# Kernel tuning notes

Hardware: AMD Instinct MI355X
Metric: run time of the kernel (lower is better)

The kernel has to match this reference:

```python
import jax, jax.numpy as jnp
import numpy as np

N, B, H, OUT, T = 200000, 1024, 256, 128, 2  # nodes, graphs, hidden(=in_dim), out_dim, timesteps
NEG_SLOPE = 0.01


def setup_inputs() -> dict:
    key = jax.random.key(0)
    ks = jax.random.split(key, 12)
    s = 0.05
    f32 = jnp.float32
    return {
        "x": jax.random.normal(ks[0], (N, H), dtype=f32),
        "batch": jnp.sort(jax.random.randint(ks[1], (N,), 0, B)),
        # GATConv params (heads=1, shared lin for src/dst since in_channels is int)
        "W": jax.random.normal(ks[2], (H, H), dtype=f32) * s,
        "att_src": jax.random.normal(ks[3], (H,), dtype=f32) * s,
        "att_dst": jax.random.normal(ks[4], (H,), dtype=f32) * s,
        "bias_gat": jnp.zeros((H,), dtype=f32),
        # GRUCell params (input_size = H, hidden_size = H)
        "W_ih": jax.random.normal(ks[5], (3 * H, H), dtype=f32) * s,
        "W_hh": jax.random.normal(ks[6], (3 * H, H), dtype=f32) * s,
        "b_ih": jnp.zeros((3 * H,), dtype=f32),
        "b_hh": jnp.zeros((3 * H,), dtype=f32),
        # final Linear
        "W_lin": jax.random.normal(ks[7], (H, OUT), dtype=f32) * s,
        "b_lin": jnp.zeros((OUT,), dtype=f32),
    }


def reference(x, batch, W, att_src, att_dst, bias_gat, W_ih, W_hh, b_ih, b_hh, W_lin, b_lin):
    # out = global_add_pool(x, batch)  -> [B, H]
    out = jax.ops.segment_sum(x, batch, num_segments=B)
    for _ in range(T):
        # --- bipartite GATConv((x, out), edge_index=[arange(N), batch]) ---
        xs = x @ W                       # [N, H] transformed source nodes
        od = out @ W                     # [B, H] transformed dst (graph) nodes
        a_src = xs @ att_src             # [N]
        a_dst = od @ att_dst             # [B]
        e = a_src + a_dst[batch]         # [N] per-edge raw score (one edge per node)
        e = jnp.where(e > 0, e, NEG_SLOPE * e)  # leaky_relu(negative_slope=0.01)
        # scatter-softmax over each graph's incoming edges
        emax = jax.ops.segment_max(e, batch, num_segments=B)
        ee = jnp.exp(e - emax[batch])
        denom = jax.ops.segment_sum(ee, batch, num_segments=B)
        alpha = ee / denom[batch]        # [N]
        # scatter-add aggregation of weighted messages
        agg = jax.ops.segment_sum(xs * alpha[:, None], batch, num_segments=B) + bias_gat
        h = jax.nn.elu(agg)              # [B, H]  (dropout is identity in eval)
        # --- GRUCell(h, out) ---
        gi = h @ W_ih.T + b_ih           # [B, 3H]
        gh = out @ W_hh.T + b_hh         # [B, 3H]
        r = jax.nn.sigmoid(gi[:, :H] + gh[:, :H])
        z = jax.nn.sigmoid(gi[:, H:2 * H] + gh[:, H:2 * H])
        n = jnp.tanh(gi[:, 2 * H:] + r * gh[:, 2 * H:])
        out = jax.nn.silu((1.0 - z) * n + z * out)  # activation = F.silu
    return out @ W_lin + b_lin           # [B, OUT]
```

## Files before the change

kernel.cpp:

```cpp
#include <hip/hip_runtime.h>
#include <math.h>

#define N_NODES 200000
#define BGRAPH  1024
#define HDIM    256
#define ODIM    128
#define SCAP    1024

typedef __attribute__((ext_vector_type(8))) short short8;
typedef __attribute__((ext_vector_type(4))) float f32x4;

__device__ __forceinline__ unsigned short f2bf(float f) {
    union { float f; unsigned int i; } c; c.f = f;
    unsigned int i = c.i;
    unsigned int r = i + 0x7FFFu + ((i >> 16) & 1u);
    return (unsigned short)(r >> 16);
}

__global__ __launch_bounds__(256) void k_prep(const float* __restrict__ W,
        const float* __restrict__ att_src, const float* __restrict__ att_dst,
        const int* __restrict__ batch, float* __restrict__ v, float* __restrict__ u,
        int* __restrict__ seg) {
    int t = threadIdx.x;
    if (blockIdx.x < 256) {
        int i = blockIdx.x;
        float w = W[(size_t)i * HDIM + t];
        __shared__ float r1[256], r2[256];
        r1[t] = w * att_src[t];
        r2[t] = w * att_dst[t];
        __syncthreads();
        for (int st = 128; st > 0; st >>= 1) {
            if (t < st) { r1[t] += r1[t + st]; r2[t] += r2[t + st]; }
            __syncthreads();
        }
        if (t == 0) { v[i] = r1[0]; u[i] = r2[0]; }
    } else {
        int b = (blockIdx.x - 256) * 256 + t;
        if (b > BGRAPH) return;
        if (b == BGRAPH) { seg[b] = N_NODES; return; }
        int lo = 0, hi = N_NODES;
        while (lo < hi) { int mid = (lo + hi) >> 1; if (batch[mid] < b) lo = mid + 1; else hi = mid; }
        seg[b] = lo;
    }
}

__global__ __launch_bounds__(256) void k_passAB(const float* __restrict__ x,
        const int* __restrict__ seg, const float* __restrict__ v,
        const float* __restrict__ u, const float* __restrict__ W,
        const float* __restrict__ bias_gat,
        float* __restrict__ s, float* __restrict__ smax,
        float* __restrict__ stt, float* __restrict__ hbuf) {
    int b = blockIdx.x;
    int lo = seg[b], hi = seg[b + 1];
    int t = threadIdx.x, wave = t >> 6, lane = t & 63;
    float v0 = v[4 * lane + 0], v1 = v[4 * lane + 1], v2 = v[4 * lane + 2], v3 = v[4 * lane + 3];
    __shared__ float s_loc[SCAP];
    __shared__ float comb[4][HDIM];
    __shared__ float red[256];
    __shared__ float sred[4], dred[4];
    bool inl = (hi - lo) <= SCAP;

    float p0 = 0.f, p1 = 0.f, p2 = 0.f, p3 = 0.f;
    float sm = -3.402823466e38f;
    int i = lo + wave;
    for (; i + 4 < hi; i += 8) {
        const float4 r0 = *(const float4*)(x + (size_t)i * HDIM + 4 * lane);
        const float4 r1 = *(const float4*)(x + (size_t)(i + 4) * HDIM + 4 * lane);
        p0 += r0.x + r1.x; p1 += r0.y + r1.y; p2 += r0.z + r1.z; p3 += r0.w + r1.w;
        float pa = r0.x * v0 + r0.y * v1 + r0.z * v2 + r0.w * v3;
        float pb = r1.x * v0 + r1.y * v1 + r1.z * v2 + r1.w * v3;
        #pragma unroll
        for (int off = 32; off > 0; off >>= 1) {
            pa += __shfl_down(pa, off, 64);
            pb += __shfl_down(pb, off, 64);
        }
        if (lane == 0) {
            s[i] = pa; s[i + 4] = pb;
            if (inl) { s_loc[i - lo] = pa; s_loc[i + 4 - lo] = pb; }
            sm = fmaxf(sm, fmaxf(pa, pb));
        }
    }
    for (; i < hi; i += 4) {
        const float4 r0 = *(const float4*)(x + (size_t)i * HDIM + 4 * lane);
        p0 += r0.x; p1 += r0.y; p2 += r0.z; p3 += r0.w;
        float pa = r0.x * v0 + r0.y * v1 + r0.z * v2 + r0.w * v3;
        #pragma unroll
        for (int off = 32; off > 0; off >>= 1) pa += __shfl_down(pa, off, 64);
        if (lane == 0) {
            s[i] = pa;
            if (inl) s_loc[i - lo] = pa;
            sm = fmaxf(sm, pa);
        }
    }
    comb[wave][4 * lane + 0] = p0; comb[wave][4 * lane + 1] = p1;
    comb[wave][4 * lane + 2] = p2; comb[wave][4 * lane + 3] = p3;
    if (lane == 0) sred[wave] = sm;
    __syncthreads();
    float st0 = comb[0][t] + comb[1][t] + comb[2][t] + comb[3][t];
    stt[(size_t)b * HDIM + t] = st0;
    float smx = fmaxf(fmaxf(sred[0], sred[1]), fmaxf(sred[2], sred[3]));
    if (t == 0) smax[b] = smx;
    red[t] = st0 * u[t];
    __syncthreads();
    for (int st = 128; st > 0; st >>= 1) { if (t < st) red[t] += red[t + st]; __syncthreads(); }
    float d1 = red[0];
    __syncthreads();
    float M = smx + d1;
    M = M > 0.f ? M : 0.01f * M;

    float a0 = 0.f, a1 = 0.f, a2 = 0.f, a3 = 0.f, den = 0.f;
    i = lo + wave;
    for (; i + 12 < hi; i += 16) {
        float s0v = inl ? s_loc[i - lo]      : s[i];
        float s1v = inl ? s_loc[i + 4 - lo]  : s[i + 4];
        float s2v = inl ? s_loc[i + 8 - lo]  : s[i + 8];
        float s3v = inl ? s_loc[i + 12 - lo] : s[i + 12];
        float e0 = s0v + d1; e0 = e0 > 0.f ? e0 : 0.01f * e0;
        float e1 = s1v + d1; e1 = e1 > 0.f ? e1 : 0.01f * e1;
        float e2 = s2v + d1; e2 = e2 > 0.f ? e2 : 0.01f * e2;
        float e3 = s3v + d1; e3 = e3 > 0.f ? e3 : 0.01f * e3;
        float w0 = __expf(e0 - M), w1 = __expf(e1 - M);
        float w2 = __expf(e2 - M), w3 = __expf(e3 - M);
        const float4 r0 = *(const float4*)(x + (size_t)i * HDIM + 4 * lane);
        const float4 r1 = *(const float4*)(x + (size_t)(i + 4) * HDIM + 4 * lane);
        const float4 r2 = *(const float4*)(x + (size_t)(i + 8) * HDIM + 4 * lane);
        const float4 r3 = *(const float4*)(x + (size_t)(i + 12) * HDIM + 4 * lane);
        den += (w0 + w1) + (w2 + w3);
        a0 += w0 * r0.x + w1 * r1.x + w2 * r2.x + w3 * r3.x;
        a1 += w0 * r0.y + w1 * r1.y + w2 * r2.y + w3 * r3.y;
        a2 += w0 * r0.z + w1 * r1.z + w2 * r2.z + w3 * r3.z;
        a3 += w0 * r0.w + w1 * r1.w + w2 * r2.w + w3 * r3.w;
    }
    for (; i < hi; i += 4) {
        float s0v = inl ? s_loc[i - lo] : s[i];
        float e0 = s0v + d1; e0 = e0 > 0.f ? e0 : 0.01f * e0;
        float w0 = __expf(e0 - M);
        const float4 r0 = *(const float4*)(x + (size_t)i * HDIM + 4 * lane);
        den += w0;
        a0 += w0 * r0.x; a1 += w0 * r0.y; a2 += w0 * r0.z; a3 += w0 * r0.w;
    }
    __syncthreads();
    comb[wave][4 * lane + 0] = a0; comb[wave][4 * lane + 1] = a1;
    comb[wave][4 * lane + 2] = a2; comb[wave][4 * lane + 3] = a3;
    if (lane == 0) dred[wave] = den;
    __syncthreads();
    float dtot = dred[0] + dred[1] + dred[2] + dred[3];
    float inv = (hi > lo) ? 1.0f / dtot : 0.f;
    __shared__ float ax[HDIM];
    ax[t] = (comb[0][t] + comb[1][t] + comb[2][t] + comb[3][t]) * inv;
    __syncthreads();
    float acc = bias_gat[t];
    #pragma unroll 8
    for (int ii = 0; ii < HDIM; ++ii) acc += ax[ii] * W[(size_t)ii * HDIM + t];
    hbuf[(size_t)b * HDIM + t] = acc > 0.f ? acc : expm1f(acc);
}

__global__ __launch_bounds__(256) void k_iter2(const float* __restrict__ x,
        const int* __restrict__ seg, const float* __restrict__ s,
        const float* __restrict__ u, const float* __restrict__ smax,
        float* __restrict__ stt,
        const float* __restrict__ gi, const float* __restrict__ gh,
        const float* __restrict__ b_ih, const float* __restrict__ b_hh,
        const float* __restrict__ W, const float* __restrict__ bias_gat,
        float* __restrict__ hbuf) {
    int b = blockIdx.x, t = threadIdx.x;
    int lo = seg[b], hi = seg[b + 1];
    size_t base = (size_t)b * (3 * HDIM);
    float gir = gi[base + t] + b_ih[t];
    float giz = gi[base + HDIM + t] + b_ih[HDIM + t];
    float gin = gi[base + 2 * HDIM + t] + b_ih[2 * HDIM + t];
    float ghr = gh[base + t] + b_hh[t];
    float ghz = gh[base + HDIM + t] + b_hh[HDIM + t];
    float ghn = gh[base + 2 * HDIM + t] + b_hh[2 * HDIM + t];
    float r = 1.f / (1.f + __expf(-(gir + ghr)));
    float z = 1.f / (1.f + __expf(-(giz + ghz)));
    float n = tanhf(gin + r * ghn);
    float prev = stt[(size_t)b * HDIM + t];
    float h2 = (1.f - z) * n + z * prev;
    float st_j = h2 / (1.f + __expf(-h2));
    stt[(size_t)b * HDIM + t] = st_j;

    __shared__ float red[256];
    red[t] = st_j * u[t];
    __syncthreads();
    for (int st = 128; st > 0; st >>= 1) { if (t < st) red[t] += red[t + st]; __syncthreads(); }
    float d2 = red[0];
    __syncthreads();
    float M = smax[b] + d2;
    M = M > 0.f ? M : 0.01f * M;

    int wave = t >> 6, lane = t & 63;
    float a0 = 0.f, a1 = 0.f, a2 = 0.f, a3 = 0.f, den = 0.f;
    int i = lo + wave;
    for (; i + 12 < hi; i += 16) {
        float e0 = s[i] + d2;      e0 = e0 > 0.f ? e0 : 0.01f * e0;
        float e1 = s[i + 4] + d2;  e1 = e1 > 0.f ? e1 : 0.01f * e1;
        float e2 = s[i + 8] + d2;  e2 = e2 > 0.f ? e2 : 0.01f * e2;
        float e3 = s[i + 12] + d2; e3 = e3 > 0.f ? e3 : 0.01f * e3;
        float w0 = __expf(e0 - M), w1 = __expf(e1 - M);
        float w2 = __expf(e2 - M), w3 = __expf(e3 - M);
        const float4 r0 = *(const float4*)(x + (size_t)i * HDIM + 4 * lane);
        const float4 r1 = *(const float4*)(x + (size_t)(i + 4) * HDIM + 4 * lane);
        const float4 r2 = *(const float4*)(x + (size_t)(i + 8) * HDIM + 4 * lane);
        const float4 r3 = *(const float4*)(x + (size_t)(i + 12) * HDIM + 4 * lane);
        den += (w0 + w1) + (w2 + w3);
        a0 += w0 * r0.x + w1 * r1.x + w2 * r2.x + w3 * r3.x;
        a1 += w0 * r0.y + w1 * r1.y + w2 * r2.y + w3 * r3.y;
        a2 += w0 * r0.z + w1 * r1.z + w2 * r2.z + w3 * r3.z;
        a3 += w0 * r0.w + w1 * r1.w + w2 * r2.w + w3 * r3.w;
    }
    for (; i < hi; i += 4) {
        float e0 = s[i] + d2; e0 = e0 > 0.f ? e0 : 0.01f * e0;
        float w0 = __expf(e0 - M);
        const float4 r0 = *(const float4*)(x + (size_t)i * HDIM + 4 * lane);
        den += w0;
        a0 += w0 * r0.x; a1 += w0 * r0.y; a2 += w0 * r0.z; a3 += w0 * r0.w;
    }
    __shared__ float comb[4][HDIM];
    __shared__ float dred[4];
    comb[wave][4 * lane + 0] = a0; comb[wave][4 * lane + 1] = a1;
    comb[wave][4 * lane + 2] = a2; comb[wave][4 * lane + 3] = a3;
    if (lane == 0) dred[wave] = den;
    __syncthreads();
    float dtot = dred[0] + dred[1] + dred[2] + dred[3];
    float inv = (hi > lo) ? 1.0f / dtot : 0.f;
    __shared__ float ax[HDIM];
    ax[t] = (comb[0][t] + comb[1][t] + comb[2][t] + comb[3][t]) * inv;
    __syncthreads();
    float acc = bias_gat[t];
    #pragma unroll 8
    for (int ii = 0; ii < HDIM; ++ii) acc += ax[ii] * W[(size_t)ii * HDIM + t];
    hbuf[(size_t)b * HDIM + t] = acc > 0.f ? acc : expm1f(acc);
}

__global__ __launch_bounds__(256) void k_gemm2m(const float* __restrict__ A0,
        const float* __restrict__ A1, const float* __restrict__ B0,
        const float* __restrict__ B1, float* __restrict__ C0, float* __restrict__ C1) {
    const int K = HDIM, N = 3 * HDIM;
    const float* A = blockIdx.z ? A1 : A0;
    const float* Bm = blockIdx.z ? B1 : B0;
    float* C = blockIdx.z ? C1 : C0;
    int m0 = blockIdx.x * 64, n0 = blockIdx.y * 64;
    __shared__ __align__(16) unsigned short As[64][40];
    __shared__ __align__(16) unsigned short Bs[64][40];
    int t = threadIdx.x;
    int wave = t >> 6, lane = t & 63;
    int quad = lane >> 4, l16 = lane & 15;
    f32x4 acc[4] = {};
    for (int k0 = 0; k0 < K; k0 += 32) {
        int r = t >> 2;
        int kq = (t & 3) << 3;
        float4 av0 = *(const float4*)(A + (size_t)(m0 + r) * K + k0 + kq);
        float4 av1 = *(const float4*)(A + (size_t)(m0 + r) * K + k0 + kq + 4);
        short8 pa;
        pa[0] = (short)f2bf(av0.x); pa[1] = (short)f2bf(av0.y);
        pa[2] = (short)f2bf(av0.z); pa[3] = (short)f2bf(av0.w);
        pa[4] = (short)f2bf(av1.x); pa[5] = (short)f2bf(av1.y);
        pa[6] = (short)f2bf(av1.z); pa[7] = (short)f2bf(av1.w);
        *(short8*)&As[r][kq] = pa;
        float4 bv0 = *(const float4*)(Bm + (size_t)(n0 + r) * K + k0 + kq);
        float4 bv1 = *(const float4*)(Bm + (size_t)(n0 + r) * K + k0 + kq + 4);
        short8 pb;
        pb[0] = (short)f2bf(bv0.x); pb[1] = (short)f2bf(bv0.y);
        pb[2] = (short)f2bf(bv0.z); pb[3] = (short)f2bf(bv0.w);
        pb[4] = (short)f2bf(bv1.x); pb[5] = (short)f2bf(bv1.y);
        pb[6] = (short)f2bf(bv1.z); pb[7] = (short)f2bf(bv1.w);
        *(short8*)&Bs[r][kq] = pb;
        __syncthreads();
        short8 a = *(const short8*)&As[wave * 16 + l16][quad * 8];
        #pragma unroll
        for (int tn = 0; tn < 4; ++tn) {
            short8 bfr = *(const short8*)&Bs[tn * 16 + l16][quad * 8];
            acc[tn] = __builtin_amdgcn_mfma_f32_16x16x32_bf16(a, bfr, acc[tn], 0, 0, 0);
        }
        __syncthreads();
    }
    #pragma unroll
    for (int tn = 0; tn < 4; ++tn)
        #pragma unroll
        for (int rr = 0; rr < 4; ++rr)
            C[(size_t)(m0 + wave * 16 + quad * 4 + rr) * N + n0 + tn * 16 + l16] = acc[tn][rr];
}

__global__ __launch_bounds__(256) void k_final(const float* __restrict__ gi,
        const float* __restrict__ gh, const float* __restrict__ b_ih,
        const float* __restrict__ b_hh, const float* __restrict__ stt,
        const float* __restrict__ B, const float* __restrict__ bias,
        float* __restrict__ C, int M, int N, int K) {
    __shared__ __align__(16) float As[16][64];
    __shared__ __align__(16) float Bs[16][64];
    int tx = threadIdx.x & 15, ty = threadIdx.x >> 4;
    int m0 = blockIdx.x * 64, n0 = blockIdx.y * 64;
    float acc[4][4] = {};
    for (int k0 = 0; k0 < K; k0 += 16) {
        {
            int r = threadIdx.x >> 2;
            int kk0 = (threadIdx.x & 3) << 2;
            int mrow = m0 + r;
            size_t base = (size_t)mrow * (3 * HDIM);
            #pragma unroll
            for (int q = 0; q < 4; ++q) {
                int k = k0 + kk0 + q;
                float gir = gi[base + k] + b_ih[k];
                float giz = gi[base + HDIM + k] + b_ih[HDIM + k];
                float gin = gi[base + 2 * HDIM + k] + b_ih[2 * HDIM + k];
                float ghr = gh[base + k] + b_hh[k];
                float ghz = gh[base + HDIM + k] + b_hh[HDIM + k];
                float ghn = gh[base + 2 * HDIM + k] + b_hh[2 * HDIM + k];
                float rg = 1.f / (1.f + __expf(-(gir + ghr)));
                float zg = 1.f / (1.f + __expf(-(giz + ghz)));
                float ng = tanhf(gin + rg * ghn);
                float prev = stt[(size_t)mrow * HDIM + k];
                float h2 = (1.f - zg) * ng + zg * prev;
                As[kk0 + q][r] = h2 / (1.f + __expf(-h2));
            }
        }
        {
            int kk = threadIdx.x >> 4;
            int nn = (threadIdx.x & 15) << 2;
            float4 bv = *(const float4*)(B + (size_t)(k0 + kk) * N + n0 + nn);
            Bs[kk][nn + 0] = bv.x; Bs[kk][nn + 1] = bv.y;
            Bs[kk][nn + 2] = bv.z; Bs[kk][nn + 3] = bv.w;
        }
        __syncthreads();
        #pragma unroll
        for (int kk = 0; kk < 16; ++kk) {
            float4 a = *(const float4*)&As[kk][ty * 4];
            float4 bb = *(const float4*)&Bs[kk][tx * 4];
            acc[0][0] += a.x * bb.x; acc[0][1] += a.x * bb.y; acc[0][2] += a.x * bb.z; acc[0][3] += a.x * bb.w;
            acc[1][0] += a.y * bb.x; acc[1][1] += a.y * bb.y; acc[1][2] += a.y * bb.z; acc[1][3] += a.y * bb.w;
            acc[2][0] += a.z * bb.x; acc[2][1] += a.z * bb.y; acc[2][2] += a.z * bb.z; acc[2][3] += a.z * bb.w;
            acc[3][0] += a.w * bb.x; acc[3][1] += a.w * bb.y; acc[3][2] += a.w * bb.z; acc[3][3] += a.w * bb.w;
        }
        __syncthreads();
    }
    float bsv[4];
    #pragma unroll
    for (int j = 0; j < 4; ++j) bsv[j] = bias[n0 + tx * 4 + j];
    #pragma unroll
    for (int i = 0; i < 4; ++i) {
        int mrow = m0 + ty * 4 + i;
        *(float4*)(C + (size_t)mrow * N + n0 + tx * 4) =
            make_float4(acc[i][0] + bsv[0], acc[i][1] + bsv[1],
                        acc[i][2] + bsv[2], acc[i][3] + bsv[3]);
    }
}

extern "C" void kernel_launch(void* const* d_in, const int* in_sizes, int n_in,
                              void* d_out, int out_size, void* d_ws, size_t ws_size,
                              hipStream_t stream) {
    const float* x        = (const float*)d_in[0];
    const int*   batch    = (const int*)d_in[1];
    const float* W        = (const float*)d_in[2];
    const float* att_src  = (const float*)d_in[3];
    const float* att_dst  = (const float*)d_in[4];
    const float* bias_gat = (const float*)d_in[5];
    const float* W_ih     = (const float*)d_in[6];
    const float* W_hh     = (const float*)d_in[7];
    const float* b_ih     = (const float*)d_in[8];
    const float* b_hh     = (const float*)d_in[9];
    const float* W_lin    = (const float*)d_in[10];
    const float* b_lin    = (const float*)d_in[11];

    char* ws = (char*)d_ws;
    size_t off = 0;
    auto alloc = [&](size_t bytes) {
        void* p = (void*)(ws + off);
        off += (bytes + 255) & ~(size_t)255;
        return p;
    };
    int*   seg  = (int*)alloc((BGRAPH + 1) * 4);
    float* vv   = (float*)alloc(HDIM * 4);
    float* uu   = (float*)alloc(HDIM * 4);
    float* smax = (float*)alloc(BGRAPH * 4);
    float* s    = (float*)alloc((size_t)N_NODES * 4);
    float* stt  = (float*)alloc((size_t)BGRAPH * HDIM * 4);
    float* hbuf = (float*)alloc((size_t)BGRAPH * HDIM * 4);
    float* gi   = (float*)alloc((size_t)BGRAPH * 3 * HDIM * 4);
    float* gh   = (float*)alloc((size_t)BGRAPH * 3 * HDIM * 4);

    hipLaunchKernelGGL(k_prep, dim3(261), dim3(256), 0, stream,
                       W, att_src, att_dst, batch, vv, uu, seg);
    hipLaunchKernelGGL(k_passAB, dim3(BGRAPH), dim3(256), 0, stream,
                       x, seg, vv, uu, W, bias_gat, s, smax, stt, hbuf);
    hipLaunchKernelGGL(k_gemm2m, dim3(BGRAPH / 64, (3 * HDIM) / 64, 2), dim3(256), 0,
                       stream, hbuf, stt, W_ih, W_hh, gi, gh);
    hipLaunchKernelGGL(k_iter2, dim3(BGRAPH), dim3(256), 0, stream,
                       x, seg, s, uu, smax, stt, gi, gh, b_ih, b_hh, W, bias_gat, hbuf);
    hipLaunchKernelGGL(k_gemm2m, dim3(BGRAPH / 64, (3 * HDIM) / 64, 2), dim3(256), 0,
                       stream, hbuf, stt, W_ih, W_hh, gi, gh);
    hipLaunchKernelGGL(k_final, dim3(BGRAPH / 64, ODIM / 64), dim3(256), 0, stream,
                       gi, gh, b_ih, b_hh, stt, W_lin, b_lin, (float*)d_out,
                       BGRAPH, ODIM, HDIM);
}
```

Before: 480.2 us.

## Fuse both GAT/GRU timesteps and final linear into one per-graph kernel

Collapses the passAB, MFMA GEMM, iter2 and final kernels into a single per-graph kernel that runs both timesteps, the GRU matvecs and the output projection in-block. The GRU weights are pre-packed into an interleaved bf16 layout in the prep kernel, and each thread does scalar dot products against them. The aim is to remove the gi/gh/stt/hbuf global round trips and four kernel launches. In exchange, each block now reads the full packed GRU weights serially with scalar FMAs instead of using MFMA tiles, which costs extra per-block compute and L2 traffic.

```diff
diff --git a/kernel.cpp b/kernel.cpp
--- a/kernel.cpp
+++ b/kernel.cpp
@@ -8,7 +8,6 @@
 #define SCAP    1024
 
 typedef __attribute__((ext_vector_type(8))) short short8;
-typedef __attribute__((ext_vector_type(4))) float f32x4;
 
 __device__ __forceinline__ unsigned short f2bf(float f) {
     union { float f; unsigned int i; } c; c.f = f;
@@ -16,11 +15,17 @@
     unsigned int r = i + 0x7FFFu + ((i >> 16) & 1u);
     return (unsigned short)(r >> 16);
 }
+__device__ __forceinline__ float bf2f(unsigned short h) {
+    union { unsigned int i; float f; } c; c.i = ((unsigned int)h) << 16;
+    return c.f;
+}
 
 __global__ __launch_bounds__(256) void k_prep(const float* __restrict__ W,
         const float* __restrict__ att_src, const float* __restrict__ att_dst,
-        const int* __restrict__ batch, float* __restrict__ v, float* __restrict__ u,
-        int* __restrict__ seg) {
+        const int* __restrict__ batch, const float* __restrict__ W_ih,
+        const float* __restrict__ W_hh, float* __restrict__ v,
+        float* __restrict__ u, int* __restrict__ seg,
+        unsigned short* __restrict__ Wg) {
     int t = threadIdx.x;
     if (blockIdx.x < 256) {
         int i = blockIdx.x;
@@ -34,32 +39,51 @@
             __syncthreads();
         }
         if (t == 0) { v[i] = r1[0]; u[i] = r2[0]; }
-    } else {
+    } else if (blockIdx.x < 261) {
         int b = (blockIdx.x - 256) * 256 + t;
         if (b > BGRAPH) return;
         if (b == BGRAPH) { seg[b] = N_NODES; return; }
         int lo = 0, hi = N_NODES;
         while (lo < hi) { int mid = (lo + hi) >> 1; if (batch[mid] < b) lo = mid + 1; else hi = mid; }
         seg[b] = lo;
-    }
-}
-
-__global__ __launch_bounds__(256) void k_passAB(const float* __restrict__ x,
+    } else {
+        int k = blockIdx.x - 261;
+        short8 w8;
+        #pragma unroll
+        for (int j = 0; j < 3; ++j)
+            w8[j] = (short)f2bf(W_ih[(size_t)(j * HDIM + t) * HDIM + k]);
+        #pragma unroll
+        for (int j = 0; j < 3; ++j)
+            w8[3 + j] = (short)f2bf(W_hh[(size_t)(j * HDIM + t) * HDIM + k]);
+        w8[6] = 0; w8[7] = 0;
+        *(short8*)(Wg + ((size_t)k * HDIM + t) * 8) = w8;
+    }
+}
+
+__global__ __launch_bounds__(256, 4) void k_fused(const float* __restrict__ x,
         const int* __restrict__ seg, const float* __restrict__ v,
         const float* __restrict__ u, const float* __restrict__ W,
-        const float* __restrict__ bias_gat,
-        float* __restrict__ s, float* __restrict__ smax,
-        float* __restrict__ stt, float* __restrict__ hbuf) {
+        const float* __restrict__ bias_gat, const unsigned short* __restrict__ Wg,
+        const float* __restrict__ b_ih, const float* __restrict__ b_hh,
+        const float* __restrict__ W_lin, const float* __restrict__ b_lin,
+        float* __restrict__ sfall, float* __restrict__ out) {
     int b = blockIdx.x;
     int lo = seg[b], hi = seg[b + 1];
     int t = threadIdx.x, wave = t >> 6, lane = t & 63;
-    float v0 = v[4 * lane + 0], v1 = v[4 * lane + 1], v2 = v[4 * lane + 2], v3 = v[4 * lane + 3];
+
     __shared__ float s_loc[SCAP];
     __shared__ float comb[4][HDIM];
     __shared__ float red[256];
+    __shared__ float axv[HDIM];
+    __shared__ float hvec[HDIM];
+    __shared__ float oprev[HDIM];
     __shared__ float sred[4], dred[4];
+
     bool inl = (hi - lo) <= SCAP;
-
+    float ut = u[t];
+
+    float v0 = v[4 * lane + 0], v1 = v[4 * lane + 1];
+    float v2 = v[4 * lane + 2], v3 = v[4 * lane + 3];
     float p0 = 0.f, p1 = 0.f, p2 = 0.f, p3 = 0.f;
     float sm = -3.402823466e38f;
     int i = lo + wave;
@@ -75,8 +99,8 @@
             pb += __shfl_down(pb, off, 64);
         }
         if (lane == 0) {
-            s[i] = pa; s[i + 4] = pb;
             if (inl) { s_loc[i - lo] = pa; s_loc[i + 4 - lo] = pb; }
+            else     { sfall[i] = pa; sfall[i + 4] = pb; }
             sm = fmaxf(sm, fmaxf(pa, pb));
         }
     }
@@ -87,8 +111,7 @@
         #pragma unroll
         for (int off = 32; off > 0; off >>= 1) pa += __shfl_down(pa, off, 64);
         if (lane == 0) {
-            s[i] = pa;
-            if (inl) s_loc[i - lo] = pa;
+            if (inl) s_loc[i - lo] = pa; else sfall[i] = pa;
             sm = fmaxf(sm, pa);
         }
     }
@@ -97,253 +120,112 @@
     if (lane == 0) sred[wave] = sm;
     __syncthreads();
     float st0 = comb[0][t] + comb[1][t] + comb[2][t] + comb[3][t];
-    stt[(size_t)b * HDIM + t] = st0;
+    oprev[t] = st0;
     float smx = fmaxf(fmaxf(sred[0], sred[1]), fmaxf(sred[2], sred[3]));
-    if (t == 0) smax[b] = smx;
-    red[t] = st0 * u[t];
+    red[t] = st0 * ut;
     __syncthreads();
     for (int st = 128; st > 0; st >>= 1) { if (t < st) red[t] += red[t + st]; __syncthreads(); }
-    float d1 = red[0];
-    __syncthreads();
-    float M = smx + d1;
-    M = M > 0.f ? M : 0.01f * M;
-
-    float a0 = 0.f, a1 = 0.f, a2 = 0.f, a3 = 0.f, den = 0.f;
-    i = lo + wave;
-    for (; i + 12 < hi; i += 16) {
-        float s0v = inl ? s_loc[i - lo]      : s[i];
-        float s1v = inl ? s_loc[i + 4 - lo]  : s[i + 4];
-        float s2v = inl ? s_loc[i + 8 - lo]  : s[i + 8];
-        float s3v = inl ? s_loc[i + 12 - lo] : s[i + 12];
-        float e0 = s0v + d1; e0 = e0 > 0.f ? e0 : 0.01f * e0;
-        float e1 = s1v + d1; e1 = e1 > 0.f ? e1 : 0.01f * e1;
-        float e2 = s2v + d1; e2 = e2 > 0.f ? e2 : 0.01f * e2;
-        float e3 = s3v + d1; e3 = e3 > 0.f ? e3 : 0.01f * e3;
-        float w0 = __expf(e0 - M), w1 = __expf(e1 - M);
-        float w2 = __expf(e2 - M), w3 = __expf(e3 - M);
-        const float4 r0 = *(const float4*)(x + (size_t)i * HDIM + 4 * lane);
-        const float4 r1 = *(const float4*)(x + (size_t)(i + 4) * HDIM + 4 * lane);
-        const float4 r2 = *(const float4*)(x + (size_t)(i + 8) * HDIM + 4 * lane);
-        const float4 r3 = *(const float4*)(x + (size_t)(i + 12) * HDIM + 4 * lane);
-        den += (w0 + w1) + (w2 + w3);
-        a0 += w0 * r0.x + w1 * r1.x + w2 * r2.x + w3 * r3.x;
-        a1 += w0 * r0.y + w1 * r1.y + w2 * r2.y + w3 * r3.y;
-        a2 += w0 * r0.z + w1 * r1.z + w2 * r2.z + w3 * r3.z;
-        a3 += w0 * r0.w + w1 * r1.w + w2 * r2.w + w3 * r3.w;
-    }
-    for (; i < hi; i += 4) {
-        float s0v = inl ? s_loc[i - lo] : s[i];
-        float e0 = s0v + d1; e0 = e0 > 0.f ? e0 : 0.01f * e0;
-        float w0 = __expf(e0 - M);
-        const float4 r0 = *(const float4*)(x + (size_t)i * HDIM + 4 * lane);
-        den += w0;
-        a0 += w0 * r0.x; a1 += w0 * r0.y; a2 += w0 * r0.z; a3 += w0 * r0.w;
-    }
-    __syncthreads();
-    comb[wave][4 * lane + 0] = a0; comb[wave][4 * lane + 1] = a1;
-    comb[wave][4 * lane + 2] = a2; comb[wave][4 * lane + 3] = a3;
-    if (lane == 0) dred[wave] = den;
-    __syncthreads();
-    float dtot = dred[0] + dred[1] + dred[2] + dred[3];
-    float inv = (hi > lo) ? 1.0f / dtot : 0.f;
-    __shared__ float ax[HDIM];
-    ax[t] = (comb[0][t] + comb[1][t] + comb[2][t] + comb[3][t]) * inv;
-    __syncthreads();
-    float acc = bias_gat[t];
+    float d = red[0];
+    __syncthreads();
+
+    for (int step = 0; step < 2; ++step) {
+        float M = smx + d;
+        M = M > 0.f ? M : 0.01f * M;
+
+        float a0 = 0.f, a1 = 0.f, a2 = 0.f, a3 = 0.f, den = 0.f;
+        i = lo + wave;
+        for (; i + 12 < hi; i += 16) {
+            float s0v = inl ? s_loc[i - lo]      : sfall[i];
+            float s1v = inl ? s_loc[i + 4 - lo]  : sfall[i + 4];
+            float s2v = inl ? s_loc[i + 8 - lo]  : sfall[i + 8];
+            float s3v = inl ? s_loc[i + 12 - lo] : sfall[i + 12];
+            float e0 = s0v + d; e0 = e0 > 0.f ? e0 : 0.01f * e0;
+            float e1 = s1v + d; e1 = e1 > 0.f ? e1 : 0.01f * e1;
+            float e2 = s2v + d; e2 = e2 > 0.f ? e2 : 0.01f * e2;
+            float e3 = s3v + d; e3 = e3 > 0.f ? e3 : 0.01f * e3;
+            float w0 = __expf(e0 - M), w1 = __expf(e1 - M);
+            float w2 = __expf(e2 - M), w3 = __expf(e3 - M);
+            const float4 r0 = *(const float4*)(x + (size_t)i * HDIM + 4 * lane);
+            const float4 r1 = *(const float4*)(x + (size_t)(i + 4) * HDIM + 4 * lane);
+            const float4 r2 = *(const float4*)(x + (size_t)(i + 8) * HDIM + 4 * lane);
+            const float4 r3 = *(const float4*)(x + (size_t)(i + 12) * HDIM + 4 * lane);
+            den += (w0 + w1) + (w2 + w3);
+            a0 += w0 * r0.x + w1 * r1.x + w2 * r2.x + w3 * r3.x;
+            a1 += w0 * r0.y + w1 * r1.y + w2 * r2.y + w3 * r3.y;
+            a2 += w0 * r0.z + w1 * r1.z + w2 * r2.z + w3 * r3.z;
+            a3 += w0 * r0.w + w1 * r1.w + w2 * r2.w + w3 * r3.w;
+        }
+        for (; i < hi; i += 4) {
+            float s0v = inl ? s_loc[i - lo] : sfall[i];
+            float e0 = s0v + d; e0 = e0 > 0.f ? e0 : 0.01f * e0;
+            float w0 = __expf(e0 - M);
+            const float4 r0 = *(const float4*)(x + (size_t)i * HDIM + 4 * lane);
+            den += w0;
+            a0 += w0 * r0.x; a1 += w0 * r0.y; a2 += w0 * r0.z; a3 += w0 * r0.w;
+        }
+        comb[wave][4 * lane + 0] = a0; comb[wave][4 * lane + 1] = a1;
+        comb[wave][4 * lane + 2] = a2; comb[wave][4 * lane + 3] = a3;
+        if (lane == 0) dred[wave] = den;
+        __syncthreads();
+        float dtot = dred[0] + dred[1] + dred[2] + dred[3];
+        float inv = (hi > lo) ? 1.0f / dtot : 0.f;
+        axv[t] = (comb[0][t] + comb[1][t] + comb[2][t] + comb[3][t]) * inv;
+        __syncthreads();
+
+        float acc = bias_gat[t];
+        #pragma unroll 8
+        for (int ii = 0; ii < HDIM; ++ii) acc += axv[ii] * W[(size_t)ii * HDIM + t];
+        float hval = acc > 0.f ? acc : expm1f(acc);
+        __syncthreads();
+        hvec[t] = hval;
+        __syncthreads();
+
+        float gr = 0.f, gz = 0.f, gn = 0.f, hr = 0.f, hz = 0.f, hn = 0.f;
+        for (int k0 = 0; k0 < HDIM; k0 += 4) {
+            float hq[4], oq[4];
+            *(float4*)hq = *(const float4*)&hvec[k0];
+            *(float4*)oq = *(const float4*)&oprev[k0];
+            #pragma unroll
+            for (int j = 0; j < 4; ++j) {
+                short8 wv = *(const short8*)(Wg + ((size_t)(k0 + j) * HDIM + t) * 8);
+                gr += hq[j] * bf2f((unsigned short)wv[0]);
+                gz += hq[j] * bf2f((unsigned short)wv[1]);
+                gn += hq[j] * bf2f((unsigned short)wv[2]);
+                hr += oq[j] * bf2f((unsigned short)wv[3]);
+                hz += oq[j] * bf2f((unsigned short)wv[4]);
+                hn += oq[j] * bf2f((unsigned short)wv[5]);
+            }
+        }
+        float gir = gr + b_ih[t];
+        float giz = gz + b_ih[HDIM + t];
+        float gin = gn + b_ih[2 * HDIM + t];
+        float ghr = hr + b_hh[t];
+        float ghz = hz + b_hh[HDIM + t];
+        float ghn = hn + b_hh[2 * HDIM + t];
+        float rg = 1.f / (1.f + __expf(-(gir + ghr)));
+        float zg = 1.f / (1.f + __expf(-(giz + ghz)));
+        float ng = tanhf(gin + rg * ghn);
+        float prev = oprev[t];
+        float h2 = (1.f - zg) * ng + zg * prev;
+        float no = h2 / (1.f + __expf(-h2));
+        __syncthreads();
+        oprev[t] = no;
+        red[t] = no * ut;
+        __syncthreads();
+        for (int st = 128; st > 0; st >>= 1) { if (t < st) red[t] += red[t + st]; __syncthreads(); }
+        d = red[0];
+        __syncthreads();
+    }
+
+    int half = t >> 7, o = t & 127;
+    float acc = 0.f;
     #pragma unroll 8
-    for (int ii = 0; ii < HDIM; ++ii) acc += ax[ii] * W[(size_t)ii * HDIM + t];
-    hbuf[(size_t)b * HDIM + t] = acc > 0.f ? acc : expm1f(acc);
-}
-
-__global__ __launch_bounds__(256) void k_iter2(const float* __restrict__ x,
-        const int* __restrict__ seg, const float* __restrict__ s,
-        const float* __restrict__ u, const float* __restrict__ smax,
-        float* __restrict__ stt,
-        const float* __restrict__ gi, const float* __restrict__ gh,
-        const float* __restrict__ b_ih, const float* __restrict__ b_hh,
-        const float* __restrict__ W, const float* __restrict__ bias_gat,
-        float* __restrict__ hbuf) {
-    int b = blockIdx.x, t = threadIdx.x;
-    int lo = seg[b], hi = seg[b + 1];
-    size_t base = (size_t)b * (3 * HDIM);
-    float gir = gi[base + t] + b_ih[t];
-    float giz = gi[base + HDIM + t] + b_ih[HDIM + t];
-    float gin = gi[base + 2 * HDIM + t] + b_ih[2 * HDIM + t];
-    float ghr = gh[base + t] + b_hh[t];
-    float ghz = gh[base + HDIM + t] + b_hh[HDIM + t];
-    float ghn = gh[base + 2 * HDIM + t] + b_hh[2 * HDIM + t];
-    float r = 1.f / (1.f + __expf(-(gir + ghr)));
-    float z = 1.f / (1.f + __expf(-(giz + ghz)));
-    float n = tanhf(gin + r * ghn);
-    float prev = stt[(size_t)b * HDIM + t];
-    float h2 = (1.f - z) * n + z * prev;
-    float st_j = h2 / (1.f + __expf(-h2));
-    stt[(size_t)b * HDIM + t] = st_j;
-
-    __shared__ float red[256];
-    red[t] = st_j * u[t];
-    __syncthreads();
-    for (int st = 128; st > 0; st >>= 1) { if (t < st) red[t] += red[t + st]; __syncthreads(); }
-    float d2 = red[0];
-    __syncthreads();
-    float M = smax[b] + d2;
-    M = M > 0.f ? M : 0.01f * M;
-
-    int wave = t >> 6, lane = t & 63;
-    float a0 = 0.f, a1 = 0.f, a2 = 0.f, a3 = 0.f, den = 0.f;
-    int i = lo + wave;
-    for (; i + 12 < hi; i += 16) {
-        float e0 = s[i] + d2;      e0 = e0 > 0.f ? e0 : 0.01f * e0;
-        float e1 = s[i + 4] + d2;  e1 = e1 > 0.f ? e1 : 0.01f * e1;
-        float e2 = s[i + 8] + d2;  e2 = e2 > 0.f ? e2 : 0.01f * e2;
-        float e3 = s[i + 12] + d2; e3 = e3 > 0.f ? e3 : 0.01f * e3;
-        float w0 = __expf(e0 - M), w1 = __expf(e1 - M);
-        float w2 = __expf(e2 - M), w3 = __expf(e3 - M);
-        const float4 r0 = *(const float4*)(x + (size_t)i * HDIM + 4 * lane);
-        const float4 r1 = *(const float4*)(x + (size_t)(i + 4) * HDIM + 4 * lane);
-        const float4 r2 = *(const float4*)(x + (size_t)(i + 8) * HDIM + 4 * lane);
-        const float4 r3 = *(const float4*)(x + (size_t)(i + 12) * HDIM + 4 * lane);
-        den += (w0 + w1) + (w2 + w3);
-        a0 += w0 * r0.x + w1 * r1.x + w2 * r2.x + w3 * r3.x;
-        a1 += w0 * r0.y + w1 * r1.y + w2 * r2.y + w3 * r3.y;
-        a2 += w0 * r0.z + w1 * r1.z + w2 * r2.z + w3 * r3.z;
-        a3 += w0 * r0.w + w1 * r1.w + w2 * r2.w + w3 * r3.w;
-    }
-    for (; i < hi; i += 4) {
-        float e0 = s[i] + d2; e0 = e0 > 0.f ? e0 : 0.01f * e0;
-        float w0 = __expf(e0 - M);
-        const float4 r0 = *(const float4*)(x + (size_t)i * HDIM + 4 * lane);
-        den += w0;
-        a0 += w0 * r0.x; a1 += w0 * r0.y; a2 += w0 * r0.z; a3 += w0 * r0.w;
-    }
-    __shared__ float comb[4][HDIM];
-    __shared__ float dred[4];
-    comb[wave][4 * lane + 0] = a0; comb[wave][4 * lane + 1] = a1;
-    comb[wave][4 * lane + 2] = a2; comb[wave][4 * lane + 3] = a3;
-    if (lane == 0) dred[wave] = den;
-    __syncthreads();
-    float dtot = dred[0] + dred[1] + dred[2] + dred[3];
-    float inv = (hi > lo) ? 1.0f / dtot : 0.f;
-    __shared__ float ax[HDIM];
-    ax[t] = (comb[0][t] + comb[1][t] + comb[2][t] + comb[3][t]) * inv;
-    __syncthreads();
-    float acc = bias_gat[t];
-    #pragma unroll 8
-    for (int ii = 0; ii < HDIM; ++ii) acc += ax[ii] * W[(size_t)ii * HDIM + t];
-    hbuf[(size_t)b * HDIM + t] = acc > 0.f ? acc : expm1f(acc);
-}
-
-__global__ __launch_bounds__(256) void k_gemm2m(const float* __restrict__ A0,
-        const float* __restrict__ A1, const float* __restrict__ B0,
-        const float* __restrict__ B1, float* __restrict__ C0, float* __restrict__ C1) {
-    const int K = HDIM, N = 3 * HDIM;
-    const float* A = blockIdx.z ? A1 : A0;
-    const float* Bm = blockIdx.z ? B1 : B0;
-    float* C = blockIdx.z ? C1 : C0;
-    int m0 = blockIdx.x * 64, n0 = blockIdx.y * 64;
-    __shared__ __align__(16) unsigned short As[64][40];
-    __shared__ __align__(16) unsigned short Bs[64][40];
-    int t = threadIdx.x;
-    int wave = t >> 6, lane = t & 63;
-    int quad = lane >> 4, l16 = lane & 15;
-    f32x4 acc[4] = {};
-    for (int k0 = 0; k0 < K; k0 += 32) {
-        int r = t >> 2;
-        int kq = (t & 3) << 3;
-        float4 av0 = *(const float4*)(A + (size_t)(m0 + r) * K + k0 + kq);
-        float4 av1 = *(const float4*)(A + (size_t)(m0 + r) * K + k0 + kq + 4);
-        short8 pa;
-        pa[0] = (short)f2bf(av0.x); pa[1] = (short)f2bf(av0.y);
-        pa[2] = (short)f2bf(av0.z); pa[3] = (short)f2bf(av0.w);
-        pa[4] = (short)f2bf(av1.x); pa[5] = (short)f2bf(av1.y);
-        pa[6] = (short)f2bf(av1.z); pa[7] = (short)f2bf(av1.w);
-        *(short8*)&As[r][kq] = pa;
-        float4 bv0 = *(const float4*)(Bm + (size_t)(n0 + r) * K + k0 + kq);
-        float4 bv1 = *(const float4*)(Bm + (size_t)(n0 + r) * K + k0 + kq + 4);
-        short8 pb;
-        pb[0] = (short)f2bf(bv0.x); pb[1] = (short)f2bf(bv0.y);
-        pb[2] = (short)f2bf(bv0.z); pb[3] = (short)f2bf(bv0.w);
-        pb[4] = (short)f2bf(bv1.x); pb[5] = (short)f2bf(bv1.y);
-        pb[6] = (short)f2bf(bv1.z); pb[7] = (short)f2bf(bv1.w);
-        *(short8*)&Bs[r][kq] = pb;
-        __syncthreads();
-        short8 a = *(const short8*)&As[wave * 16 + l16][quad * 8];
-        #pragma unroll
-        for (int tn = 0; tn < 4; ++tn) {
-            short8 bfr = *(const short8*)&Bs[tn * 16 + l16][quad * 8];
-            acc[tn] = __builtin_amdgcn_mfma_f32_16x16x32_bf16(a, bfr, acc[tn], 0, 0, 0);
-        }
-        __syncthreads();
-    }
-    #pragma unroll
-    for (int tn = 0; tn < 4; ++tn)
-        #pragma unroll
-        for (int rr = 0; rr < 4; ++rr)
-            C[(size_t)(m0 + wave * 16 + quad * 4 + rr) * N + n0 + tn * 16 + l16] = acc[tn][rr];
-}
-
-__global__ __launch_bounds__(256) void k_final(const float* __restrict__ gi,
-        const float* __restrict__ gh, const float* __restrict__ b_ih,
-        const float* __restrict__ b_hh, const float* __restrict__ stt,
-        const float* __restrict__ B, const float* __restrict__ bias,
-        float* __restrict__ C, int M, int N, int K) {
-    __shared__ __align__(16) float As[16][64];
-    __shared__ __align__(16) float Bs[16][64];
-    int tx = threadIdx.x & 15, ty = threadIdx.x >> 4;
-    int m0 = blockIdx.x * 64, n0 = blockIdx.y * 64;
-    float acc[4][4] = {};
-    for (int k0 = 0; k0 < K; k0 += 16) {
-        {
-            int r = threadIdx.x >> 2;
-            int kk0 = (threadIdx.x & 3) << 2;
-            int mrow = m0 + r;
-            size_t base = (size_t)mrow * (3 * HDIM);
-            #pragma unroll
-            for (int q = 0; q < 4; ++q) {
-                int k = k0 + kk0 + q;
-                float gir = gi[base + k] + b_ih[k];
-                float giz = gi[base + HDIM + k] + b_ih[HDIM + k];
-                float gin = gi[base + 2 * HDIM + k] + b_ih[2 * HDIM + k];
-                float ghr = gh[base + k] + b_hh[k];
-                float ghz = gh[base + HDIM + k] + b_hh[HDIM + k];
-                float ghn = gh[base + 2 * HDIM + k] + b_hh[2 * HDIM + k];
-                float rg = 1.f / (1.f + __expf(-(gir + ghr)));
-                float zg = 1.f / (1.f + __expf(-(giz + ghz)));
-                float ng = tanhf(gin + rg * ghn);
-                float prev = stt[(size_t)mrow * HDIM + k];
-                float h2 = (1.f - zg) * ng + zg * prev;
-                As[kk0 + q][r] = h2 / (1.f + __expf(-h2));
-            }
-        }
-        {
-            int kk = threadIdx.x >> 4;
-            int nn = (threadIdx.x & 15) << 2;
-            float4 bv = *(const float4*)(B + (size_t)(k0 + kk) * N + n0 + nn);
-            Bs[kk][nn + 0] = bv.x; Bs[kk][nn + 1] = bv.y;
-            Bs[kk][nn + 2] = bv.z; Bs[kk][nn + 3] = bv.w;
-        }
-        __syncthreads();
-        #pragma unroll
-        for (int kk = 0; kk < 16; ++kk) {
-            float4 a = *(const float4*)&As[kk][ty * 4];
-            float4 bb = *(const float4*)&Bs[kk][tx * 4];
-            acc[0][0] += a.x * bb.x; acc[0][1] += a.x * bb.y; acc[0][2] += a.x * bb.z; acc[0][3] += a.x * bb.w;
-            acc[1][0] += a.y * bb.x; acc[1][1] += a.y * bb.y; acc[1][2] += a.y * bb.z; acc[1][3] += a.y * bb.w;
-            acc[2][0] += a.z * bb.x; acc[2][1] += a.z * bb.y; acc[2][2] += a.z * bb.z; acc[2][3] += a.z * bb.w;
-            acc[3][0] += a.w * bb.x; acc[3][1] += a.w * bb.y; acc[3][2] += a.w * bb.z; acc[3][3] += a.w * bb.w;
-        }
-        __syncthreads();
-    }
-    float bsv[4];
-    #pragma unroll
-    for (int j = 0; j < 4; ++j) bsv[j] = bias[n0 + tx * 4 + j];
-    #pragma unroll
-    for (int i = 0; i < 4; ++i) {
-        int mrow = m0 + ty * 4 + i;
-        *(float4*)(C + (size_t)mrow * N + n0 + tx * 4) =
-            make_float4(acc[i][0] + bsv[0], acc[i][1] + bsv[1],
-                        acc[i][2] + bsv[2], acc[i][3] + bsv[3]);
-    }
+    for (int k = 0; k < 128; ++k)
+        acc += oprev[half * 128 + k] * W_lin[(size_t)(half * 128 + k) * ODIM + o];
+    red[t] = acc;
+    __syncthreads();
+    if (t < 128)
+        out[(size_t)b * ODIM + t] = red[t] + red[t + 128] + b_lin[t];
 }
 
 extern "C" void kernel_launch(void* const* d_in, const int* in_sizes, int n_in,
@@ -369,27 +251,15 @@
         off += (bytes + 255) & ~(size_t)255;
         return p;
     };
-    int*   seg  = (int*)alloc((BGRAPH + 1) * 4);
-    float* vv   = (float*)alloc(HDIM * 4);
-    float* uu   = (float*)alloc(HDIM * 4);
-    float* smax = (float*)alloc(BGRAPH * 4);
-    float* s    = (float*)alloc((size_t)N_NODES * 4);
-    float* stt  = (float*)alloc((size_t)BGRAPH * HDIM * 4);
-    float* hbuf = (float*)alloc((size_t)BGRAPH * HDIM * 4);
-    float* gi   = (float*)alloc((size_t)BGRAPH * 3 * HDIM * 4);
-    float* gh   = (float*)alloc((size_t)BGRAPH * 3 * HDIM * 4);
-
-    hipLaunchKernelGGL(k_prep, dim3(261), dim3(256), 0, stream,
-                       W, att_src, att_dst, batch, vv, uu, seg);
-    hipLaunchKernelGGL(k_passAB, dim3(BGRAPH), dim3(256), 0, stream,
-                       x, seg, vv, uu, W, bias_gat, s, smax, stt, hbuf);
-    hipLaunchKernelGGL(k_gemm2m, dim3(BGRAPH / 64, (3 * HDIM) / 64, 2), dim3(256), 0,
-                       stream, hbuf, stt, W_ih, W_hh, gi, gh);
-    hipLaunchKernelGGL(k_iter2, dim3(BGRAPH), dim3(256), 0, stream,
-                       x, seg, s, uu, smax, stt, gi, gh, b_ih, b_hh, W, bias_gat, hbuf);
-    hipLaunchKernelGGL(k_gemm2m, dim3(BGRAPH / 64, (3 * HDIM) / 64, 2), dim3(256), 0,
-                       stream, hbuf, stt, W_ih, W_hh, gi, gh);
-    hipLaunchKernelGGL(k_final, dim3(BGRAPH / 64, ODIM / 64), dim3(256), 0, stream,
-                       gi, gh, b_ih, b_hh, stt, W_lin, b_lin, (float*)d_out,
-                       BGRAPH, ODIM, HDIM);
-}
+    int*            seg   = (int*)alloc((BGRAPH + 1) * 4);
+    float*          vv    = (float*)alloc(HDIM * 4);
+    float*          uu    = (float*)alloc(HDIM * 4);
+    float*          sfall = (float*)alloc((size_t)N_NODES * 4);
+    unsigned short* Wg    = (unsigned short*)alloc((size_t)HDIM * HDIM * 8 * 2);
+
+    hipLaunchKernelGGL(k_prep, dim3(517), dim3(256), 0, stream,
+                       W, att_src, att_dst, batch, W_ih, W_hh, vv, uu, seg, Wg);
+    hipLaunchKernelGGL(k_fused, dim3(BGRAPH), dim3(256), 0, stream,
+                       x, seg, vv, uu, W, bias_gat, Wg, b_ih, b_hh,
+                       W_lin, b_lin, sfall, (float*)d_out);
+}
```

Result: faster. 444.4 us (-7.4%).
